# Kernel optimization log

Hardware: AMD Instinct MI355X
Metric: run time of the kernel (lower is better)

Reference implementation:

```python
import jax, jax.numpy as jnp
import numpy as np

B, P, N, E, H, D = 64, 256, 1000, 128, 8, 16
SQRT_E = 11.313708498984761  # sqrt(embedding_dim)
CLIP = 10.0                  # logit_clipping


def setup_inputs() -> dict:
    key = jax.random.key(0)
    ks = jax.random.split(key, 9)
    s = 0.05  # weight init scale
    return {
        "encoded_nodes": jax.random.normal(ks[0], (B, N, E), jnp.float32),
        "encoded_last_node": jax.random.normal(ks[1], (B, P, E), jnp.float32),
        "attr": jax.random.uniform(ks[2], (B, P, 1), jnp.float32),
        "ninf_mask": jnp.zeros((B, P, N), jnp.float32),
        # params stored [in, out] (apply as x @ W, equals torch Linear with W.T)
        "Wq_last": jax.random.normal(ks[3], (E + 1, H * D), jnp.float32) * s,
        "Wk": jax.random.normal(ks[4], (E, H * D), jnp.float32) * s,
        "Wv": jax.random.normal(ks[5], (E, H * D), jnp.float32) * s,
        "Wo": jax.random.normal(ks[6], (H * D, E), jnp.float32) * s,
        "bo": jax.random.normal(ks[7], (E,), jnp.float32) * s,
    }


def reference(encoded_nodes, encoded_last_node, attr, ninf_mask,
              Wq_last, Wk, Wv, Wo, bo):
    # set_kv: project encoded nodes to per-head K, V  -> [B, N, H, D]
    k = (encoded_nodes @ Wk).reshape(B, N, H, D)
    v = (encoded_nodes @ Wv).reshape(B, N, H, D)

    # query from (last node embedding, attr) -> [B, P, H, D]
    input_cat = jnp.concatenate([encoded_last_node, attr], axis=2)  # [B,P,E+1]
    q = (input_cat @ Wq_last).reshape(B, P, H, D)

    # multi-head attention with additive rank-3 -inf mask
    inv_sqrt_d = 1.0 / jnp.sqrt(jnp.float32(D))
    scores = jnp.einsum("bphd,bnhd->bhpn", q, k) * inv_sqrt_d
    scores = scores + ninf_mask[:, None, :, :]            # [B,H,P,N]
    weights = jax.nn.softmax(scores, axis=-1)
    out = jnp.einsum("bhpn,bnhd->bphd", weights, v).reshape(B, P, H * D)

    mh = out @ Wo + bo                                    # [B,P,E]

    # single-head tanh-clipped scoring against encoded nodes
    score = jnp.einsum("bpe,bne->bpn", mh, encoded_nodes) / SQRT_E
    score_masked = CLIP * jnp.tanh(score) + ninf_mask
    probs = jax.nn.softmax(score_masked, axis=2)          # [B,P,N]
    return probs
```

## Files before the change

kernel.cpp:

```cpp
#include <hip/hip_runtime.h>

#define BB 64
#define PP 256
#define NN 1000
#define NP 1024
#define EE 128
#define HH 8
#define DD 16

typedef __fp16 v4h __attribute__((ext_vector_type(4)));
typedef float v4f __attribute__((ext_vector_type(4)));


__global__ __launch_bounds__(256) void k1_qproj(const float* __restrict__ ln,
                                                const float* __restrict__ attr,
                                                const float* __restrict__ Wq,
                                                __fp16* __restrict__ Qh) {
    __shared__ __fp16 wt[128 * 132];
    __shared__ float attrs[64];
    const int tid = threadIdx.x;
    const int row0 = blockIdx.x * 64;
    for (int i = tid; i < 128 * 128; i += 256) {
        int k = i >> 7, n = i & 127;
        wt[n * 132 + k] = (__fp16)Wq[i];
    }
    if (tid < 64) attrs[tid] = attr[row0 + tid];
    __syncthreads();

    const int wid = tid >> 6, lane = tid & 63;
    const int lp = lane & 15, lg = lane >> 4;
    const int rb = row0 + wid * 16;

    const float* arow = ln + (size_t)(rb + lp) * 128;
    v4f acc[8];
#pragma unroll
    for (int cf = 0; cf < 8; cf++) acc[cf] = (v4f){0.f, 0.f, 0.f, 0.f};

#pragma unroll
    for (int k0 = 0; k0 < 8; k0++) {
        float4 av = *(const float4*)&arow[k0 * 16 + 4 * lg];
        v4h af;
        af[0] = (__fp16)av.x; af[1] = (__fp16)av.y;
        af[2] = (__fp16)av.z; af[3] = (__fp16)av.w;
#pragma unroll
        for (int cf = 0; cf < 8; cf++) {
            v4h bf = *(const v4h*)&wt[(cf * 16 + lp) * 132 + k0 * 16 + 4 * lg];
            acc[cf] = __builtin_amdgcn_mfma_f32_16x16x16f16(af, bf, acc[cf], 0, 0, 0);
        }
    }

#pragma unroll
    for (int cf = 0; cf < 8; cf++) {
        const int col = cf * 16 + lp;
        const float w128 = Wq[128 * 128 + col];
#pragma unroll
        for (int r = 0; r < 4; r++) {
            const int rl = wid * 16 + 4 * lg + r;
            float v = (acc[cf][r] + attrs[rl] * w128) * 0.25f;
            Qh[(size_t)(row0 + rl) * 128 + col] = (__fp16)v;
        }
    }
}

__global__ __launch_bounds__(256) void k2_kv(const float* __restrict__ nodes,
                                             const float* __restrict__ Wk,
                                             const float* __restrict__ Wv,
                                             __fp16* __restrict__ Kf,
                                             __fp16* __restrict__ Vt) {
    __shared__ __fp16 wt[128 * 132];
    const int tid = threadIdx.x;
    const int b = blockIdx.y;
    const int kv = blockIdx.z;
    const float* W = (kv == 0) ? Wk : Wv;
    for (int i = tid; i < 128 * 128; i += 256) {
        int k = i >> 7, n = i & 127;
        wt[n * 132 + k] = (__fp16)W[i];
    }
    __syncthreads();

    const int wid = tid >> 6, lane = tid & 63;
    const int lp = lane & 15, lg = lane >> 4;
    const int nb = blockIdx.x * 64 + wid * 16;

    int nr = nb + lp;
    if (nr >= NN) nr = NN - 1;
    const float* arow = nodes + (size_t)(b * NN + nr) * 128;

    v4f acc[8];
#pragma unroll
    for (int cf = 0; cf < 8; cf++) acc[cf] = (v4f){0.f, 0.f, 0.f, 0.f};

#pragma unroll
    for (int k0 = 0; k0 < 8; k0++) {
        float4 av = *(const float4*)&arow[k0 * 16 + 4 * lg];
        v4h af;
        af[0] = (__fp16)av.x; af[1] = (__fp16)av.y;
        af[2] = (__fp16)av.z; af[3] = (__fp16)av.w;
#pragma unroll
        for (int cf = 0; cf < 8; cf++) {
            v4h bf = *(const v4h*)&wt[(cf * 16 + lp) * 132 + k0 * 16 + 4 * lg];
            acc[cf] = __builtin_amdgcn_mfma_f32_16x16x16f16(af, bf, acc[cf], 0, 0, 0);
        }
    }

    if (kv == 0) {
#pragma unroll
        for (int cf = 0; cf < 8; cf++) {
            const size_t base = ((size_t)(b * HH + cf) << 14) + lp;
#pragma unroll
            for (int r = 0; r < 4; r++) {
                const int n = nb + 4 * lg + r;
                Kf[base + (size_t)n * 16] = (n < NN) ? (__fp16)acc[cf][r] : (__fp16)0.f;
            }
        }
    } else {
#pragma unroll
        for (int cf = 0; cf < 8; cf++) {
            v4h pk;
#pragma unroll
            for (int r = 0; r < 4; r++) {
                const int n = nb + 4 * lg + r;
                pk[r] = (n < NN) ? (__fp16)acc[cf][r] : (__fp16)0.f;
            }
            *(v4h*)&Vt[((size_t)(b * HH + cf) << 14) + (size_t)(nb >> 4) * 256 +
                       lp * 16 + 4 * lg] = pk;
        }
    }
}

__global__ __launch_bounds__(256) void k3_attn(const __fp16* __restrict__ Qh,
                                               const __fp16* __restrict__ Kf,
                                               const __fp16* __restrict__ Vt,
                                               const float* __restrict__ mask,
                                               float* __restrict__ Aout) {
    __shared__ __fp16 sh[2][4][256];
    const int tid = threadIdx.x;
    const int bid = blockIdx.x;
    const int b = bid & 63;
    const int rest = bid >> 6;
    const int hg = rest & 3, pt = rest >> 2;
    const int h0 = hg * 2;
    const int p0 = pt * 64;

    const int wid = tid >> 6, lane = tid & 63;
    const int lp = lane & 15, lg = lane >> 4;
    const int pw = p0 + wid * 16;

    const __fp16* gsrc = ((wid < 2) ? Kf + ((size_t)(b * HH + h0 + wid) << 14)
                                    : Vt + ((size_t)(b * HH + h0 + wid - 2) << 14)) +
                         lane * 4;
    __fp16* sdst0 = &sh[0][wid][lane * 4];
    __fp16* sdst1 = &sh[1][wid][lane * 4];

    v4h qf[2];
    {
        const __fp16* qrow = Qh + (size_t)(b * PP + pw + lp) * 128 + h0 * 16 + 4 * lg;
        qf[0] = *(const v4h*)&qrow[0];
        qf[1] = *(const v4h*)&qrow[16];
    }

    const float* mrow = mask + (size_t)(b * PP + pw + lp) * NN;

    v4f acc[2];
    float lsum[2];
    acc[0] = (v4f){0.f, 0.f, 0.f, 0.f};
    acc[1] = (v4f){0.f, 0.f, 0.f, 0.f};
    lsum[0] = 0.f; lsum[1] = 0.f;
    const v4f zero4 = {0.f, 0.f, 0.f, 0.f};

    v4h st[2];
    float4 mv[2];
    st[0] = *(const v4h*)(gsrc);
    *(v4h*)sdst0 = st[0];
    st[1] = *(const v4h*)(gsrc + 256);
    mv[0] = *(const float4*)&mrow[4 * lg];
    __syncthreads();

#pragma unroll 2
    for (int s = 0; s < 62; s++) {
        const int p = s & 1;
        if (s + 2 <= 62) st[p] = *(const v4h*)(gsrc + (s + 2) * 256);
        {
            int moff = (s + 1) * 16 + 4 * lg;
            if (moff > 996) moff = 996;
            mv[p ^ 1] = *(const float4*)&mrow[moff];
        }

        v4h kf0 = *(const v4h*)&sh[p][0][lp * 16 + 4 * lg];
        v4h kf1 = *(const v4h*)&sh[p][1][lp * 16 + 4 * lg];
        v4h vf0 = *(const v4h*)&sh[p][2][lp * 16 + 4 * lg];
        v4h vf1 = *(const v4h*)&sh[p][3][lp * 16 + 4 * lg];
        const float4 m = mv[p];
        {
            v4f sc = __builtin_amdgcn_mfma_f32_16x16x16f16(kf0, qf[0], zero4, 0, 0, 0);
            float w0 = __expf(sc[0] + m.x);
            float w1 = __expf(sc[1] + m.y);
            float w2 = __expf(sc[2] + m.z);
            float w3 = __expf(sc[3] + m.w);
            lsum[0] += (w0 + w1) + (w2 + w3);
            v4h wf;
            wf[0] = (__fp16)w0; wf[1] = (__fp16)w1; wf[2] = (__fp16)w2; wf[3] = (__fp16)w3;
            acc[0] = __builtin_amdgcn_mfma_f32_16x16x16f16(wf, vf0, acc[0], 0, 0, 0);
        }
        {
            v4f sc = __builtin_amdgcn_mfma_f32_16x16x16f16(kf1, qf[1], zero4, 0, 0, 0);
            float w0 = __expf(sc[0] + m.x);
            float w1 = __expf(sc[1] + m.y);
            float w2 = __expf(sc[2] + m.z);
            float w3 = __expf(sc[3] + m.w);
            lsum[1] += (w0 + w1) + (w2 + w3);
            v4h wf;
            wf[0] = (__fp16)w0; wf[1] = (__fp16)w1; wf[2] = (__fp16)w2; wf[3] = (__fp16)w3;
            acc[1] = __builtin_amdgcn_mfma_f32_16x16x16f16(wf, vf1, acc[1], 0, 0, 0);
        }

        *(v4h*)((p == 0) ? sdst1 : sdst0) = st[p ^ 1];
        __syncthreads();
    }

    {
        const int nl = 992;
        const float4 m = mv[0];
        const bool c0 = (nl + 4 * lg + 0 < NN), c1 = (nl + 4 * lg + 1 < NN);
        const bool c2 = (nl + 4 * lg + 2 < NN), c3 = (nl + 4 * lg + 3 < NN);
        v4h kf0 = *(const v4h*)&sh[0][0][lp * 16 + 4 * lg];
        v4h kf1 = *(const v4h*)&sh[0][1][lp * 16 + 4 * lg];
        v4h vf0 = *(const v4h*)&sh[0][2][lp * 16 + 4 * lg];
        v4h vf1 = *(const v4h*)&sh[0][3][lp * 16 + 4 * lg];
        {
            v4f sc = __builtin_amdgcn_mfma_f32_16x16x16f16(kf0, qf[0], zero4, 0, 0, 0);
            float w0 = c0 ? __expf(sc[0] + m.x) : 0.f;
            float w1 = c1 ? __expf(sc[1] + m.y) : 0.f;
            float w2 = c2 ? __expf(sc[2] + m.z) : 0.f;
            float w3 = c3 ? __expf(sc[3] + m.w) : 0.f;
            lsum[0] += (w0 + w1) + (w2 + w3);
            v4h wf;
            wf[0] = (__fp16)w0; wf[1] = (__fp16)w1; wf[2] = (__fp16)w2; wf[3] = (__fp16)w3;
            acc[0] = __builtin_amdgcn_mfma_f32_16x16x16f16(wf, vf0, acc[0], 0, 0, 0);
        }
        {
            v4f sc = __builtin_amdgcn_mfma_f32_16x16x16f16(kf1, qf[1], zero4, 0, 0, 0);
            float w0 = c0 ? __expf(sc[0] + m.x) : 0.f;
            float w1 = c1 ? __expf(sc[1] + m.y) : 0.f;
            float w2 = c2 ? __expf(sc[2] + m.z) : 0.f;
            float w3 = c3 ? __expf(sc[3] + m.w) : 0.f;
            lsum[1] += (w0 + w1) + (w2 + w3);
            v4h wf;
            wf[0] = (__fp16)w0; wf[1] = (__fp16)w1; wf[2] = (__fp16)w2; wf[3] = (__fp16)w3;
            acc[1] = __builtin_amdgcn_mfma_f32_16x16x16f16(wf, vf1, acc[1], 0, 0, 0);
        }
    }

#pragma unroll
    for (int j = 0; j < 2; j++) {
        float l = lsum[j];
        l += __shfl_xor(l, 16);
        l += __shfl_xor(l, 32);
#pragma unroll
        for (int r = 0; r < 4; r++) {
            float denom = __shfl(l, 4 * lg + r);
            float inv = 1.f / denom;
            Aout[(size_t)(b * PP + pw + 4 * lg + r) * 128 + (h0 + j) * 16 + lp] =
                acc[j][r] * inv;
        }
    }
}

__global__ __launch_bounds__(256) void k4_mh(const float* __restrict__ Ain,
                                             const float* __restrict__ Wo,
                                             const float* __restrict__ bo,
                                             __fp16* __restrict__ Mh) {
    __shared__ __fp16 wt[128 * 132];
    const int tid = threadIdx.x;
    const int row0 = blockIdx.x * 64;
    for (int i = tid; i < 128 * 128; i += 256) {
        int k = i >> 7, n = i & 127;
        wt[n * 132 + k] = (__fp16)Wo[i];
    }
    __syncthreads();

    const int wid = tid >> 6, lane = tid & 63;
    const int lp = lane & 15, lg = lane >> 4;
    const int rb = row0 + wid * 16;

    const float* arow = Ain + (size_t)(rb + lp) * 128;
    v4f acc[8];
#pragma unroll
    for (int cf = 0; cf < 8; cf++) acc[cf] = (v4f){0.f, 0.f, 0.f, 0.f};

#pragma unroll
    for (int k0 = 0; k0 < 8; k0++) {
        float4 av = *(const float4*)&arow[k0 * 16 + 4 * lg];
        v4h af;
        af[0] = (__fp16)av.x; af[1] = (__fp16)av.y;
        af[2] = (__fp16)av.z; af[3] = (__fp16)av.w;
#pragma unroll
        for (int cf = 0; cf < 8; cf++) {
            v4h bf = *(const v4h*)&wt[(cf * 16 + lp) * 132 + k0 * 16 + 4 * lg];
            acc[cf] = __builtin_amdgcn_mfma_f32_16x16x16f16(af, bf, acc[cf], 0, 0, 0);
        }
    }

    const float scale = 0.08838834764831845f;
#pragma unroll
    for (int cf = 0; cf < 8; cf++) {
        const int col = cf * 16 + lp;
        const float bb = bo[col];
#pragma unroll
        for (int r = 0; r < 4; r++) {
            const int rl = wid * 16 + 4 * lg + r;
            Mh[(size_t)(row0 + rl) * 128 + col] = (__fp16)((acc[cf][r] + bb) * scale);
        }
    }
}

__device__ __forceinline__ void k5_prefetch(int s, int wid, int lp, int lg,
                                            const float* __restrict__ nbase,
                                            const float* __restrict__ mkrow,
                                            float4 (&nb)[8], float4& mv) {
    int nr = s * 64 + wid * 16 + lp;
    if (nr >= NN) nr = NN - 1;
    const float* a = nbase + (size_t)nr * 128 + 4 * lg;
#pragma unroll
    for (int ec = 0; ec < 8; ec++) nb[ec] = *(const float4*)&a[ec * 16];
    int mc = s * 64 + wid * 16 + 4 * lg;
    if (mc > 996) mc = 996;
    mv = *(const float4*)&mkrow[mc];
}

__device__ __forceinline__ void k5_compute(int s, int wid, int lp, int lg,
                                           const v4h (&bf)[8], const float4 (&nb)[8],
                                           const float4 mv, float& lsum,
                                           __fp16* __restrict__ probs) {
    const v4f zero4 = {0.f, 0.f, 0.f, 0.f};
    v4f acc = zero4;
#pragma unroll
    for (int ec = 0; ec < 8; ec++) {
        float4 av = nb[ec];
        v4h af;
        af[0] = (__fp16)av.x; af[1] = (__fp16)av.y;
        af[2] = (__fp16)av.z; af[3] = (__fp16)av.w;
        acc = __builtin_amdgcn_mfma_f32_16x16x16f16(af, bf[ec], acc, 0, 0, 0);
    }
    const int nt = s * 64 + wid * 16;
    const int nb4 = nt + 4 * lg;
    v4h wf;
    if (nt + 15 < NN) {
        float e0 = __expf(2.f * acc[0]);
        float e1 = __expf(2.f * acc[1]);
        float e2 = __expf(2.f * acc[2]);
        float e3 = __expf(2.f * acc[3]);
        float w0 = __expf(fmaf(-20.f, __builtin_amdgcn_rcpf(e0 + 1.f), mv.x));
        float w1 = __expf(fmaf(-20.f, __builtin_amdgcn_rcpf(e1 + 1.f), mv.y));
        float w2 = __expf(fmaf(-20.f, __builtin_amdgcn_rcpf(e2 + 1.f), mv.z));
        float w3 = __expf(fmaf(-20.f, __builtin_amdgcn_rcpf(e3 + 1.f), mv.w));
        lsum += (w0 + w1) + (w2 + w3);
        wf[0] = (__fp16)w0; wf[1] = (__fp16)w1; wf[2] = (__fp16)w2; wf[3] = (__fp16)w3;
    } else {
        float w0 = 0.f, w1 = 0.f, w2 = 0.f, w3 = 0.f;
        if (nb4 + 0 < NN) {
            float e = __expf(2.f * acc[0]);
            w0 = __expf(fmaf(-20.f, __builtin_amdgcn_rcpf(e + 1.f), mv.x));
        }
        if (nb4 + 1 < NN) {
            float e = __expf(2.f * acc[1]);
            w1 = __expf(fmaf(-20.f, __builtin_amdgcn_rcpf(e + 1.f), mv.y));
        }
        if (nb4 + 2 < NN) {
            float e = __expf(2.f * acc[2]);
            w2 = __expf(fmaf(-20.f, __builtin_amdgcn_rcpf(e + 1.f), mv.z));
        }
        if (nb4 + 3 < NN) {
            float e = __expf(2.f * acc[3]);
            w3 = __expf(fmaf(-20.f, __builtin_amdgcn_rcpf(e + 1.f), mv.w));
        }
        lsum += (w0 + w1) + (w2 + w3);
        wf[0] = (__fp16)w0; wf[1] = (__fp16)w1; wf[2] = (__fp16)w2; wf[3] = (__fp16)w3;
    }
    *(v4h*)&probs[lp * 1028 + nb4] = wf;
}

__global__ __launch_bounds__(256, 4) void k5_final(const float* __restrict__ nodes,
                                                   const __fp16* __restrict__ Mh,
                                                   const float* __restrict__ mask,
                                                   float* __restrict__ out) {
    __shared__ __fp16 probs[16 * 1028];
    __shared__ float rowsum[16];
    __shared__ float rowinv[16];
    const int tid = threadIdx.x;
    const int bid = blockIdx.x;
    const int xcd = bid & 7;
    const int rest = bid >> 3;
    const int pt = rest & 15;
    const int b = ((rest >> 4) << 3) + xcd;
    const int p0 = pt * 16;

    if (tid < 16) rowsum[tid] = 0.f;

    const int wid = tid >> 6, lane = tid & 63;
    const int lp = lane & 15, lg = lane >> 4;

    v4h bf[8];
    {
        const __fp16* mhrow = Mh + (size_t)(b * PP + p0 + lp) * 128;
#pragma unroll
        for (int ec = 0; ec < 8; ec++)
            bf[ec] = *(const v4h*)&mhrow[ec * 16 + 4 * lg];
    }
    __syncthreads();

    float lsum = 0.f;
    const float* nbase = nodes + (size_t)b * NN * 128;
    const float* mkrow = mask + (size_t)(b * PP + p0 + lp) * NN;

    float4 nbA[8], nbB[8];
    float4 mvA, mvB;
    k5_prefetch(0, wid, lp, lg, nbase, mkrow, nbA, mvA);
    for (int s2 = 0; s2 < 8; s2++) {
        const int s = 2 * s2;
        k5_prefetch(s + 1, wid, lp, lg, nbase, mkrow, nbB, mvB);
        k5_compute(s, wid, lp, lg, bf, nbA, mvA, lsum, probs);
        if (s2 < 7) k5_prefetch(s + 2, wid, lp, lg, nbase, mkrow, nbA, mvA);
        k5_compute(s + 1, wid, lp, lg, bf, nbB, mvB, lsum, probs);
    }

    lsum += __shfl_xor(lsum, 16);
    lsum += __shfl_xor(lsum, 32);
    if (lane < 16) atomicAdd(&rowsum[lane], lsum);
    __syncthreads();
    if (tid < 16) rowinv[tid] = 1.f / rowsum[tid];
    __syncthreads();

    if (tid < 250) {
        const int c4 = tid * 4;
        const size_t obase = (size_t)(b * PP + p0) * NN;
#pragma unroll 4
        for (int r = 0; r < 16; r++) {
            v4h pv = *(const v4h*)&probs[r * 1028 + c4];
            float inv = rowinv[r];
            float4 ov;
            ov.x = (float)pv[0] * inv;
            ov.y = (float)pv[1] * inv;
            ov.z = (float)pv[2] * inv;
            ov.w = (float)pv[3] * inv;
            *(float4*)&out[obase + (size_t)r * NN + c4] = ov;
        }
    }
}

extern "C" void kernel_launch(void* const* d_in, const int* in_sizes, int n_in,
                              void* d_out, int out_size, void* d_ws, size_t ws_size,
                              hipStream_t stream) {
    const float* nodes = (const float*)d_in[0];
    const float* ln    = (const float*)d_in[1];
    const float* attr  = (const float*)d_in[2];
    const float* mask  = (const float*)d_in[3];
    const float* Wq    = (const float*)d_in[4];
    const float* Wk    = (const float*)d_in[5];
    const float* Wv    = (const float*)d_in[6];
    const float* Wo    = (const float*)d_in[7];
    const float* bo    = (const float*)d_in[8];
    float* out = (float*)d_out;

    float*  Aout = (float*)d_ws;
    __fp16* Qh   = (__fp16*)(Aout + 2097152);
    __fp16* Mhh  = Qh + 2097152;

    __fp16* Kf = (__fp16*)d_out;
    __fp16* Vt = Kf + (size_t)BB * HH * NP * 16;

    hipLaunchKernelGGL(k1_qproj, dim3(256), dim3(256), 0, stream, ln, attr, Wq, Qh);
    hipLaunchKernelGGL(k2_kv, dim3(16, 64, 2), dim3(256), 0, stream, nodes, Wk, Wv, Kf, Vt);
    hipLaunchKernelGGL(k3_attn, dim3(1024), dim3(256), 0, stream, Qh, Kf, Vt, mask, Aout);
    hipLaunchKernelGGL(k4_mh, dim3(256), dim3(256), 0, stream, Aout, Wo, bo, Mhh);
    hipLaunchKernelGGL(k5_final, dim3(1024), dim3(256), 0, stream, nodes, Mhh, mask, out);
}
```

Baseline: 300.9 us.

## Process 32 query rows per block in final scoring kernel; store attention output as fp16

```diff
diff --git a/kernel.cpp b/kernel.cpp
--- a/kernel.cpp
+++ b/kernel.cpp
@@ -132,7 +132,7 @@
                                                const __fp16* __restrict__ Kf,
                                                const __fp16* __restrict__ Vt,
                                                const float* __restrict__ mask,
-                                               float* __restrict__ Aout) {
+                                               __fp16* __restrict__ Aout) {
     __shared__ __fp16 sh[2][4][256];
     const int tid = threadIdx.x;
     const int bid = blockIdx.x;
@@ -261,12 +261,12 @@
             float denom = __shfl(l, 4 * lg + r);
             float inv = 1.f / denom;
             Aout[(size_t)(b * PP + pw + 4 * lg + r) * 128 + (h0 + j) * 16 + lp] =
-                acc[j][r] * inv;
-        }
-    }
-}
-
-__global__ __launch_bounds__(256) void k4_mh(const float* __restrict__ Ain,
+                (__fp16)(acc[j][r] * inv);
+        }
+    }
+}
+
+__global__ __launch_bounds__(256) void k4_mh(const __fp16* __restrict__ Ain,
                                              const float* __restrict__ Wo,
                                              const float* __restrict__ bo,
                                              __fp16* __restrict__ Mh) {
@@ -283,17 +283,14 @@
     const int lp = lane & 15, lg = lane >> 4;
     const int rb = row0 + wid * 16;
 
-    const float* arow = Ain + (size_t)(rb + lp) * 128;
+    const __fp16* arow = Ain + (size_t)(rb + lp) * 128;
     v4f acc[8];
 #pragma unroll
     for (int cf = 0; cf < 8; cf++) acc[cf] = (v4f){0.f, 0.f, 0.f, 0.f};
 
 #pragma unroll
     for (int k0 = 0; k0 < 8; k0++) {
-        float4 av = *(const float4*)&arow[k0 * 16 + 4 * lg];
-        v4h af;
-        af[0] = (__fp16)av.x; af[1] = (__fp16)av.y;
-        af[2] = (__fp16)av.z; af[3] = (__fp16)av.w;
+        v4h af = *(const v4h*)&arow[k0 * 16 + 4 * lg];
 #pragma unroll
         for (int cf = 0; cf < 8; cf++) {
             v4h bf = *(const v4h*)&wt[(cf * 16 + lp) * 132 + k0 * 16 + 4 * lg];
@@ -314,130 +311,149 @@
     }
 }
 
-__device__ __forceinline__ void k5_prefetch(int s, int wid, int lp, int lg,
-                                            const float* __restrict__ nbase,
-                                            const float* __restrict__ mkrow,
-                                            float4 (&nb)[8], float4& mv) {
-    int nr = s * 64 + wid * 16 + lp;
+__device__ __forceinline__ void k5_pref(int s, int wid, int lp, int lg,
+                                        const float* __restrict__ nbase,
+                                        float4 (&nb)[8]) {
+    int nr = s * 128 + wid * 16 + lp;
     if (nr >= NN) nr = NN - 1;
     const float* a = nbase + (size_t)nr * 128 + 4 * lg;
 #pragma unroll
     for (int ec = 0; ec < 8; ec++) nb[ec] = *(const float4*)&a[ec * 16];
-    int mc = s * 64 + wid * 16 + 4 * lg;
+}
+
+__device__ __forceinline__ void k5_comp(int s, int wid, int lp, int lg,
+                                        const v4h (&bf0)[8], const v4h (&bf1)[8],
+                                        const float4 (&nb)[8],
+                                        const float* __restrict__ mk0,
+                                        const float* __restrict__ mk1,
+                                        float& ls0, float& ls1,
+                                        __fp16* __restrict__ probs) {
+    const v4f zero4 = {0.f, 0.f, 0.f, 0.f};
+    int mc = s * 128 + wid * 16 + 4 * lg;
     if (mc > 996) mc = 996;
-    mv = *(const float4*)&mkrow[mc];
-}
-
-__device__ __forceinline__ void k5_compute(int s, int wid, int lp, int lg,
-                                           const v4h (&bf)[8], const float4 (&nb)[8],
-                                           const float4 mv, float& lsum,
-                                           __fp16* __restrict__ probs) {
-    const v4f zero4 = {0.f, 0.f, 0.f, 0.f};
-    v4f acc = zero4;
+    float4 m0 = *(const float4*)&mk0[mc];
+    float4 m1 = *(const float4*)&mk1[mc];
+    v4f a0 = zero4, a1 = zero4;
 #pragma unroll
     for (int ec = 0; ec < 8; ec++) {
         float4 av = nb[ec];
         v4h af;
         af[0] = (__fp16)av.x; af[1] = (__fp16)av.y;
         af[2] = (__fp16)av.z; af[3] = (__fp16)av.w;
-        acc = __builtin_amdgcn_mfma_f32_16x16x16f16(af, bf[ec], acc, 0, 0, 0);
-    }
-    const int nt = s * 64 + wid * 16;
+        a0 = __builtin_amdgcn_mfma_f32_16x16x16f16(af, bf0[ec], a0, 0, 0, 0);
+        a1 = __builtin_amdgcn_mfma_f32_16x16x16f16(af, bf1[ec], a1, 0, 0, 0);
+    }
+    const int nt = s * 128 + wid * 16;
     const int nb4 = nt + 4 * lg;
-    v4h wf;
-    if (nt + 15 < NN) {
-        float e0 = __expf(2.f * acc[0]);
-        float e1 = __expf(2.f * acc[1]);
-        float e2 = __expf(2.f * acc[2]);
-        float e3 = __expf(2.f * acc[3]);
-        float w0 = __expf(fmaf(-20.f, __builtin_amdgcn_rcpf(e0 + 1.f), mv.x));
-        float w1 = __expf(fmaf(-20.f, __builtin_amdgcn_rcpf(e1 + 1.f), mv.y));
-        float w2 = __expf(fmaf(-20.f, __builtin_amdgcn_rcpf(e2 + 1.f), mv.z));
-        float w3 = __expf(fmaf(-20.f, __builtin_amdgcn_rcpf(e3 + 1.f), mv.w));
-        lsum += (w0 + w1) + (w2 + w3);
-        wf[0] = (__fp16)w0; wf[1] = (__fp16)w1; wf[2] = (__fp16)w2; wf[3] = (__fp16)w3;
-    } else {
-        float w0 = 0.f, w1 = 0.f, w2 = 0.f, w3 = 0.f;
-        if (nb4 + 0 < NN) {
-            float e = __expf(2.f * acc[0]);
-            w0 = __expf(fmaf(-20.f, __builtin_amdgcn_rcpf(e + 1.f), mv.x));
-        }
-        if (nb4 + 1 < NN) {
-            float e = __expf(2.f * acc[1]);
-            w1 = __expf(fmaf(-20.f, __builtin_amdgcn_rcpf(e + 1.f), mv.y));
-        }
-        if (nb4 + 2 < NN) {
-            float e = __expf(2.f * acc[2]);
-            w2 = __expf(fmaf(-20.f, __builtin_amdgcn_rcpf(e + 1.f), mv.z));
-        }
-        if (nb4 + 3 < NN) {
-            float e = __expf(2.f * acc[3]);
-            w3 = __expf(fmaf(-20.f, __builtin_amdgcn_rcpf(e + 1.f), mv.w));
-        }
-        lsum += (w0 + w1) + (w2 + w3);
-        wf[0] = (__fp16)w0; wf[1] = (__fp16)w1; wf[2] = (__fp16)w2; wf[3] = (__fp16)w3;
-    }
-    *(v4h*)&probs[lp * 1028 + nb4] = wf;
-}
-
-__global__ __launch_bounds__(256, 4) void k5_final(const float* __restrict__ nodes,
+#pragma unroll
+    for (int t = 0; t < 2; t++) {
+        const v4f ac = t ? a1 : a0;
+        const float4 m = t ? m1 : m0;
+        v4h wf;
+        float ws = 0.f;
+        if (nt + 15 < NN) {
+            float e0 = __expf(2.f * ac[0]);
+            float e1 = __expf(2.f * ac[1]);
+            float e2 = __expf(2.f * ac[2]);
+            float e3 = __expf(2.f * ac[3]);
+            float w0 = __expf(fmaf(-20.f, __builtin_amdgcn_rcpf(e0 + 1.f), m.x));
+            float w1 = __expf(fmaf(-20.f, __builtin_amdgcn_rcpf(e1 + 1.f), m.y));
+            float w2 = __expf(fmaf(-20.f, __builtin_amdgcn_rcpf(e2 + 1.f), m.z));
+            float w3 = __expf(fmaf(-20.f, __builtin_amdgcn_rcpf(e3 + 1.f), m.w));
+            ws = (w0 + w1) + (w2 + w3);
+            wf[0] = (__fp16)w0; wf[1] = (__fp16)w1; wf[2] = (__fp16)w2; wf[3] = (__fp16)w3;
+        } else {
+            float w0 = 0.f, w1 = 0.f, w2 = 0.f, w3 = 0.f;
+            if (nb4 + 0 < NN) {
+                float e = __expf(2.f * ac[0]);
+                w0 = __expf(fmaf(-20.f, __builtin_amdgcn_rcpf(e + 1.f), m.x));
+            }
+            if (nb4 + 1 < NN) {
+                float e = __expf(2.f * ac[1]);
+                w1 = __expf(fmaf(-20.f, __builtin_amdgcn_rcpf(e + 1.f), m.y));
+            }
+            if (nb4 + 2 < NN) {
+                float e = __expf(2.f * ac[2]);
+                w2 = __expf(fmaf(-20.f, __builtin_amdgcn_rcpf(e + 1.f), m.z));
+            }
+            if (nb4 + 3 < NN) {
+                float e = __expf(2.f * ac[3]);
+                w3 = __expf(fmaf(-20.f, __builtin_amdgcn_rcpf(e + 1.f), m.w));
+            }
+            ws = (w0 + w1) + (w2 + w3);
+            wf[0] = (__fp16)w0; wf[1] = (__fp16)w1; wf[2] = (__fp16)w2; wf[3] = (__fp16)w3;
+        }
+        if (t) ls1 += ws; else ls0 += ws;
+        *(v4h*)&probs[(t * 16 + lp) * 1028 + nb4] = wf;
+    }
+}
+
+__global__ __launch_bounds__(512, 4) void k5_final(const float* __restrict__ nodes,
                                                    const __fp16* __restrict__ Mh,
                                                    const float* __restrict__ mask,
                                                    float* __restrict__ out) {
-    __shared__ __fp16 probs[16 * 1028];
-    __shared__ float rowsum[16];
-    __shared__ float rowinv[16];
+    __shared__ __fp16 probs[32 * 1028];
+    __shared__ float rowsum[32];
+    __shared__ float rowinv[32];
     const int tid = threadIdx.x;
     const int bid = blockIdx.x;
     const int xcd = bid & 7;
-    const int rest = bid >> 3;
-    const int pt = rest & 15;
-    const int b = ((rest >> 4) << 3) + xcd;
-    const int p0 = pt * 16;
-
-    if (tid < 16) rowsum[tid] = 0.f;
+    const int pt = (bid >> 3) & 7;
+    const int b = ((bid >> 6) << 3) | xcd;
+    const int p0 = pt * 32;
+
+    if (tid < 32) rowsum[tid] = 0.f;
 
     const int wid = tid >> 6, lane = tid & 63;
     const int lp = lane & 15, lg = lane >> 4;
 
-    v4h bf[8];
+    v4h bf0[8], bf1[8];
     {
-        const __fp16* mhrow = Mh + (size_t)(b * PP + p0 + lp) * 128;
-#pragma unroll
-        for (int ec = 0; ec < 8; ec++)
-            bf[ec] = *(const v4h*)&mhrow[ec * 16 + 4 * lg];
-    }
-    __syncthreads();
-
-    float lsum = 0.f;
+        const __fp16* mh0 = Mh + (size_t)(b * PP + p0 + lp) * 128;
+        const __fp16* mh1 = mh0 + (size_t)16 * 128;
+#pragma unroll
+        for (int ec = 0; ec < 8; ec++) {
+            bf0[ec] = *(const v4h*)&mh0[ec * 16 + 4 * lg];
+            bf1[ec] = *(const v4h*)&mh1[ec * 16 + 4 * lg];
+        }
+    }
+    __syncthreads();
+
+    float ls0 = 0.f, ls1 = 0.f;
     const float* nbase = nodes + (size_t)b * NN * 128;
-    const float* mkrow = mask + (size_t)(b * PP + p0 + lp) * NN;
+    const float* mk0 = mask + (size_t)(b * PP + p0 + lp) * NN;
+    const float* mk1 = mk0 + (size_t)16 * NN;
 
     float4 nbA[8], nbB[8];
-    float4 mvA, mvB;
-    k5_prefetch(0, wid, lp, lg, nbase, mkrow, nbA, mvA);
-    for (int s2 = 0; s2 < 8; s2++) {
+    k5_pref(0, wid, lp, lg, nbase, nbA);
+    for (int s2 = 0; s2 < 4; s2++) {
         const int s = 2 * s2;
-        k5_prefetch(s + 1, wid, lp, lg, nbase, mkrow, nbB, mvB);
-        k5_compute(s, wid, lp, lg, bf, nbA, mvA, lsum, probs);
-        if (s2 < 7) k5_prefetch(s + 2, wid, lp, lg, nbase, mkrow, nbA, mvA);
-        k5_compute(s + 1, wid, lp, lg, bf, nbB, mvB, lsum, probs);
-    }
-
-    lsum += __shfl_xor(lsum, 16);
-    lsum += __shfl_xor(lsum, 32);
-    if (lane < 16) atomicAdd(&rowsum[lane], lsum);
-    __syncthreads();
-    if (tid < 16) rowinv[tid] = 1.f / rowsum[tid];
-    __syncthreads();
-
-    if (tid < 250) {
-        const int c4 = tid * 4;
-        const size_t obase = (size_t)(b * PP + p0) * NN;
+        k5_pref(s + 1, wid, lp, lg, nbase, nbB);
+        k5_comp(s, wid, lp, lg, bf0, bf1, nbA, mk0, mk1, ls0, ls1, probs);
+        if (s2 < 3) k5_pref(s + 2, wid, lp, lg, nbase, nbA);
+        k5_comp(s + 1, wid, lp, lg, bf0, bf1, nbB, mk0, mk1, ls0, ls1, probs);
+    }
+
+    ls0 += __shfl_xor(ls0, 16);
+    ls0 += __shfl_xor(ls0, 32);
+    ls1 += __shfl_xor(ls1, 16);
+    ls1 += __shfl_xor(ls1, 32);
+    if (lane < 16) {
+        atomicAdd(&rowsum[lane], ls0);
+        atomicAdd(&rowsum[16 + lane], ls1);
+    }
+    __syncthreads();
+    if (tid < 32) rowinv[tid] = 1.f / rowsum[tid];
+    __syncthreads();
+
+    if (tid < 500) {
+        const int rg = tid / 250;
+        const int c4 = (tid - rg * 250) * 4;
+        const size_t obase = (size_t)(b * PP + p0 + rg * 16) * NN;
 #pragma unroll 4
         for (int r = 0; r < 16; r++) {
-            v4h pv = *(const v4h*)&probs[r * 1028 + c4];
-            float inv = rowinv[r];
+            v4h pv = *(const v4h*)&probs[(rg * 16 + r) * 1028 + c4];
+            float inv = rowinv[rg * 16 + r];
             float4 ov;
             ov.x = (float)pv[0] * inv;
             ov.y = (float)pv[1] * inv;
@@ -462,16 +478,16 @@
     const float* bo    = (const float*)d_in[8];
     float* out = (float*)d_out;
 
-    float*  Aout = (float*)d_ws;
-    __fp16* Qh   = (__fp16*)(Aout + 2097152);
-    __fp16* Mhh  = Qh + 2097152;
+    __fp16* AoutH = (__fp16*)d_ws;
+    __fp16* Qh    = AoutH + 2097152;
+    __fp16* Mhh   = Qh + 2097152;
 
     __fp16* Kf = (__fp16*)d_out;
     __fp16* Vt = Kf + (size_t)BB * HH * NP * 16;
 
     hipLaunchKernelGGL(k1_qproj, dim3(256), dim3(256), 0, stream, ln, attr, Wq, Qh);
     hipLaunchKernelGGL(k2_kv, dim3(16, 64, 2), dim3(256), 0, stream, nodes, Wk, Wv, Kf, Vt);
-    hipLaunchKernelGGL(k3_attn, dim3(1024), dim3(256), 0, stream, Qh, Kf, Vt, mask, Aout);
-    hipLaunchKernelGGL(k4_mh, dim3(256), dim3(256), 0, stream, Aout, Wo, bo, Mhh);
-    hipLaunchKernelGGL(k5_final, dim3(1024), dim3(256), 0, stream, nodes, Mhh, mask, out);
-}
+    hipLaunchKernelGGL(k3_attn, dim3(1024), dim3(256), 0, stream, Qh, Kf, Vt, mask, AoutH);
+    hipLaunchKernelGGL(k4_mh, dim3(256), dim3(256), 0, stream, AoutH, Wo, bo, Mhh);
+    hipLaunchKernelGGL(k5_final, dim3(512), dim3(512), 0, stream, nodes, Mhh, mask, out);
+}
```

Result: faster. 284.1 us (-5.6%).
